# Performance work log

Measured on AMD Instinct MI355X. Metric: run time of the kernel, lower is better.

## Reference

```python
import jax, jax.numpy as jnp
import numpy as np

# SH constants (standard 3DGS eval_sh, degree 3)
C0 = 0.28209479177387814
C1 = 0.4886025119029199
C2 = (1.0925484305920792, -1.0925484305920792, 0.31539156525252005, -1.0925484305920792, 0.5462742152960396)
C3 = (-0.5900435899266435, 2.890611442640554, -0.4570457994644658, 0.3731763325901154, -0.4570457994644658, 1.445305721320277, -0.5900435899266435)

N_GAUSS = 4096
N_PTS = 32768
CHUNK = 4096  # math-identical to torch's 16384 chunking (pure concat of independent points)


def quat_to_rot(q):
    # q: (N,4) normalized, (w,x,y,z) as in 3DGS build_rotation
    r, x, y, z = q[:, 0], q[:, 1], q[:, 2], q[:, 3]
    R = jnp.stack([
        jnp.stack([1 - 2 * (y * y + z * z), 2 * (x * y - r * z), 2 * (x * z + r * y)], -1),
        jnp.stack([2 * (x * y + r * z), 1 - 2 * (x * x + z * z), 2 * (y * z - r * x)], -1),
        jnp.stack([2 * (x * z - r * y), 2 * (y * z + r * x), 1 - 2 * (x * x + y * y)], -1),
    ], axis=-2)  # (N,3,3)
    return R


def eval_sh3(sh, dirs):
    # sh: (N,16) scalar SH coeffs; dirs: (C,N,3) unit directions -> (C,N)
    x, y, z = dirs[..., 0], dirs[..., 1], dirs[..., 2]
    xx, yy, zz = x * x, y * y, z * z
    xy, yz, xz = x * y, y * z, x * z
    s = sh[None]  # (1,N,16)
    res = C0 * s[..., 0]
    res = res - C1 * y * s[..., 1] + C1 * z * s[..., 2] - C1 * x * s[..., 3]
    res = (res + C2[0] * xy * s[..., 4] + C2[1] * yz * s[..., 5]
           + C2[2] * (2 * zz - xx - yy) * s[..., 6]
           + C2[3] * xz * s[..., 7] + C2[4] * (xx - yy) * s[..., 8])
    res = (res + C3[0] * y * (3 * xx - yy) * s[..., 9] + C3[1] * xy * z * s[..., 10]
           + C3[2] * y * (4 * zz - xx - yy) * s[..., 11]
           + C3[3] * z * (2 * zz - 3 * xx - 3 * yy) * s[..., 12]
           + C3[4] * x * (4 * zz - xx - yy) * s[..., 13]
           + C3[5] * z * (xx - yy) * s[..., 14]
           + C3[6] * x * (xx - yy - 3 * zz) * s[..., 15])
    return res


def setup_inputs() -> dict:
    key = jax.random.key(0)
    ks = jax.random.split(key, 9)
    return {
        "network_pts": jax.random.normal(ks[0], (N_PTS, 3), jnp.float32),
        "network_view": jax.random.normal(ks[1], (N_PTS, 3), jnp.float32),
        "network_tx": jax.random.normal(ks[2], (N_PTS, 3), jnp.float32),
        "xyz": jax.random.normal(ks[3], (N_GAUSS, 3), jnp.float32),
        "sh_dc": jax.random.normal(ks[4], (N_GAUSS, 1), jnp.float32),
        "sh_rest": 0.1 * jax.random.normal(ks[5], (N_GAUSS, 15), jnp.float32),
        "scaling": jnp.float32(-3.0) + 0.2 * jax.random.normal(ks[6], (N_GAUSS, 3), jnp.float32),
        "rotation": jax.random.normal(ks[7], (N_GAUSS, 4), jnp.float32),
        "opacity_logit": jax.random.normal(ks[8], (N_GAUSS, 1), jnp.float32),
    }


def reference(network_pts, network_view, network_tx, xyz, sh_dc, sh_rest, scaling, rotation, opacity_logit):
    # activations, matching GaussianModel.setup_functions
    sh = jnp.concatenate([sh_dc, sh_rest], axis=1)            # (N,16)
    s = jnp.exp(scaling)                                      # (N,3)
    q = rotation / jnp.linalg.norm(rotation, axis=1, keepdims=True)
    R = quat_to_rot(q)                                        # (N,3,3)
    # precision = (L L^T)^{-1} with L = R diag(s)  =>  R diag(1/s^2) R^T
    prec = jnp.einsum('nij,nj,nkj->nik', R, 1.0 / (s * s), R)  # (N,3,3)
    op = jax.nn.sigmoid(opacity_logit)[:, 0]                  # (N,)

    pts = network_pts.reshape(-1, CHUNK, 3)

    def chunk_fn(p):  # p: (C,3)
        diff = p[:, None, :] - xyz[None, :, :]                # (C,N,3)
        maha = jnp.einsum('cni,nij,cnj->cn', diff, prec, diff)
        w = op[None, :] * jnp.exp(-0.5 * maha)                # (C,N)
        # dir_pp = xyz - query_point, normalized (as in get_magnitude)
        dirs = -diff / jnp.linalg.norm(diff, axis=-1, keepdims=True)
        mag = jnp.maximum(eval_sh3(sh, dirs), 0.0)            # (C,N)
        return w.sum(axis=1), (w * mag).sum(axis=1)

    opac_c, sig_c = jax.lax.map(chunk_fn, pts)
    return opac_c.reshape(-1), sig_c.reshape(-1)
```

## Files before the change

### kernel.cpp

```cpp
#include <hip/hip_runtime.h>
#include <hip/hip_bf16.h>

#define N_GAUSS 4096
#define N_PTS   32768
#define BLOCK   256
#define NSPLIT  32
#define SEGSZ   (N_GAUSS / NSPLIT)
#define NBLK_PT 128
#define GSTRIDE 32
#define NCELL   4096
#define NBIN    16

#define SH_C0  0.28209479177387814f
#define SH_C1  0.4886025119029199f

#define WS_GP     0
#define WS_GHIST  131072
#define WS_CELLID 135168
#define WS_SPTS   167936
#define WS_ACC    299008
#define WS_HPART  364544

__device__ __forceinline__ int cell_of(float x, float y, float z) {
    int cx = min(15, max(0, (int)((x + 3.2f) * 2.5f)));
    int cy = min(15, max(0, (int)((y + 3.2f) * 2.5f)));
    int cz = min(15, max(0, (int)((z + 3.2f) * 2.5f)));
    int ex = (cx & 1) | ((cx & 2) << 2) | ((cx & 4) << 4) | ((cx & 8) << 6);
    int ey = (cy & 1) | ((cy & 2) << 2) | ((cy & 4) << 4) | ((cy & 8) << 6);
    int ez = (cz & 1) | ((cz & 2) << 2) | ((cz & 4) << 4) | ((cz & 8) << 6);
    return ex | (ey << 1) | (ez << 2);
}

__global__ __launch_bounds__(1024) void binprep_kernel(
    const float* __restrict__ pts, const float* __restrict__ xyz,
    const float* __restrict__ sh_dc, const float* __restrict__ sh_rest,
    const float* __restrict__ scaling, const float* __restrict__ rotation,
    const float* __restrict__ opl, float* __restrict__ gp,
    int* __restrict__ cellid, int* __restrict__ hpart, float* __restrict__ acc)
{
    const int t = threadIdx.x, bx = blockIdx.x;

    if (bx >= 20) {
        float4* a4 = (float4*)acc;
        int base = (bx - 20) * 1024 * 8 + t;
        #pragma unroll
        for (int i = 0; i < 8; ++i) a4[base + i * 1024] = make_float4(0.f, 0.f, 0.f, 0.f);
        return;
    }
    if (bx >= 16) {
        int g = (bx - 16) * 1024 + t;
        float s0 = scaling[3*g+0], s1 = scaling[3*g+1], s2 = scaling[3*g+2];
        float i0 = __expf(-2.0f * s0);
        float i1 = __expf(-2.0f * s1);
        float i2 = __expf(-2.0f * s2);
        float maxs2 = __expf(2.0f * fmaxf(s0, fmaxf(s1, s2)));

        float r = rotation[4*g+0], x = rotation[4*g+1];
        float y = rotation[4*g+2], z = rotation[4*g+3];
        float n = rsqrtf(r*r + x*x + y*y + z*z);
        r *= n; x *= n; y *= n; z *= n;
        float R00 = 1.f - 2.f*(y*y + z*z), R01 = 2.f*(x*y - r*z), R02 = 2.f*(x*z + r*y);
        float R10 = 2.f*(x*y + r*z), R11 = 1.f - 2.f*(x*x + z*z), R12 = 2.f*(y*z - r*x);
        float R20 = 2.f*(x*z - r*y), R21 = 2.f*(y*z + r*x), R22 = 1.f - 2.f*(x*x + y*y);

        float pxx = 0.5f*(R00*R00*i0 + R01*R01*i1 + R02*R02*i2);
        float pxy = 0.5f*(R00*R10*i0 + R01*R11*i1 + R02*R12*i2);
        float pxz = 0.5f*(R00*R20*i0 + R01*R21*i1 + R02*R22*i2);
        float pyy = 0.5f*(R10*R10*i0 + R11*R11*i1 + R12*R12*i2);
        float pyz = 0.5f*(R10*R20*i0 + R11*R21*i1 + R12*R22*i2);
        float pzz = 0.5f*(R20*R20*i0 + R21*R21*i1 + R22*R22*i2);

        float op   = 1.f / (1.f + __expf(-opl[g]));
        float lnop = __logf(op);
        float Tg   = 2.0f * maxs2 * (lnop + 16.0f);

        float* G = gp + (size_t)g * GSTRIDE;
        G[0] = xyz[3*g+0]; G[1] = xyz[3*g+1]; G[2] = xyz[3*g+2]; G[3] = Tg;
        G[4] = pxx; G[5] = pxy; G[6] = pxz; G[7] = pyy;
        G[8] = pyz; G[9] = pzz; G[10] = lnop; G[11] = 0.f;

        const float* sr = sh_rest + (size_t)g * 15;
        G[12] =  SH_C0 * sh_dc[g];
        G[13] = -SH_C1 * sr[0];
        G[14] =  SH_C1 * sr[1];
        G[15] = -SH_C1 * sr[2];
        G[16] =  1.0925484305920792f  * sr[3];
        G[17] = -1.0925484305920792f  * sr[4];
        G[18] =  0.31539156525252005f * sr[5];
        G[19] = -1.0925484305920792f  * sr[6];
        G[20] =  0.5462742152960396f  * sr[7];
        G[21] = -0.5900435899266435f  * sr[8];
        G[22] =  2.890611442640554f   * sr[9];
        G[23] = -0.4570457994644658f  * sr[10];
        G[24] =  0.3731763325901154f  * sr[11];
        G[25] = -0.4570457994644658f  * sr[12];
        G[26] =  1.445305721320277f   * sr[13];
        G[27] = -0.5900435899266435f  * sr[14];
        G[28] = 0.f; G[29] = 0.f; G[30] = 0.f; G[31] = 0.f;
        return;
    }

    __shared__ int s_hist[NCELL];
    #pragma unroll
    for (int i = 0; i < 4; ++i) s_hist[t + i * 1024] = 0;
    __syncthreads();
    #pragma unroll
    for (int k = 0; k < 2; ++k) {
        int p = bx * 2048 + k * 1024 + t;
        float x = pts[3*p+0], y = pts[3*p+1], z = pts[3*p+2];
        int cell = cell_of(x, y, z);
        cellid[p] = cell;
        atomicAdd(&s_hist[cell], 1);
    }
    __syncthreads();
    #pragma unroll
    for (int i = 0; i < 4; ++i) {
        int c = t + i * 1024;
        hpart[bx * NCELL + c] = s_hist[c];
    }
}

__global__ __launch_bounds__(1024) void scan_kernel(
    const int* __restrict__ hpart, int* __restrict__ ghist)
{
    __shared__ int s_scan[1024];
    const int t = threadIdx.x;
    int b = t * 4;
    int c0 = 0, c1 = 0, c2 = 0, c3 = 0;
    #pragma unroll
    for (int k = 0; k < NBIN; ++k) {
        const int* hp = hpart + k * NCELL + b;
        c0 += hp[0]; c1 += hp[1]; c2 += hp[2]; c3 += hp[3];
    }
    int s = c0 + c1 + c2 + c3;
    s_scan[t] = s;
    __syncthreads();
    for (int off = 1; off < 1024; off <<= 1) {
        int v = (t >= off) ? s_scan[t - off] : 0;
        __syncthreads();
        s_scan[t] += v;
        __syncthreads();
    }
    int excl = s_scan[t] - s;
    ghist[b]   = excl;
    ghist[b+1] = excl + c0;
    ghist[b+2] = excl + c0 + c1;
    ghist[b+3] = excl + c0 + c1 + c2;
}

__global__ __launch_bounds__(256) void scatter_kernel(
    const float* __restrict__ pts, const int* __restrict__ cellid,
    int* __restrict__ ghist, float4* __restrict__ spts)
{
    int p = blockIdx.x * 256 + threadIdx.x;
    float x = pts[3*p+0], y = pts[3*p+1], z = pts[3*p+2];
    int pos = atomicAdd(&ghist[cellid[p]], 1);
    spts[pos] = make_float4(x, y, z, __int_as_float(p));
}

__device__ __forceinline__ void eval_one(
    const float4* R, float dx, float dy, float dz, float d2,
    float& opac, float& sig)
{
    float4 q1 = R[1], q2 = R[2];
    float vx = q1.x*dx + q1.y*dy + q1.z*dz;
    float vy = q1.y*dx + q1.w*dy + q2.x*dz;
    float vz = q1.z*dx + q2.x*dy + q2.y*dz;
    float maha = dx*vx + dy*vy + dz*vz;
    float w = __expf(q2.z - maha);
    opac += w;

    if (__any(w > 1e-9f)) {
        float4 q3 = R[3], q4 = R[4], q5 = R[5], q6 = R[6];
        float rinv = rsqrtf(d2);
        float x = -dx * rinv, y = -dy * rinv, z = -dz * rinv;
        float xx = x*x, yy = y*y, zz = z*z;
        float xy = x*y, yz = y*z, xz = x*z;

        float res = q3.x;
        res += y * q3.y;
        res += z * q3.z;
        res += x * q3.w;
        res += xy * q4.x;
        res += yz * q4.y;
        res += (3.f*zz - 1.f) * q4.z;
        res += xz * q4.w;
        float xxmyy = xx - yy;
        res += xxmyy * q5.x;
        res += y * (3.f*xx - yy) * q5.y;
        res += (xy * z) * q5.z;
        float f5z1 = 5.f*zz - 1.f;
        res += y * f5z1 * q5.w;
        res += z * (5.f*zz - 3.f) * q6.x;
        res += x * f5z1 * q6.y;
        res += z * xxmyy * q6.z;
        res += x * (xxmyy - 3.f*zz) * q6.w;

        sig += w * fmaxf(res, 0.f);
    }
}

__global__ __launch_bounds__(BLOCK, 4) void gauss_kernel(
    const float4* __restrict__ spts, const float4* __restrict__ gp4,
    float* __restrict__ acc)
{
    __shared__ float s_min[4][3], s_max[4][3];
    __shared__ int s_nact;
    __shared__ int s_act[SEGSZ];
    __shared__ float4 s_rec[SEGSZ * 8];

    const int tid = threadIdx.x;
    const int pb  = blockIdx.x;
    const int seg = blockIdx.y;
    float4 P = spts[pb * 256 + tid];
    const float px = P.x, py = P.y, pz = P.z;

    float mnx = px, mxx = px, mny = py, mxy = py, mnz = pz, mxz = pz;
    #pragma unroll
    for (int off = 32; off >= 1; off >>= 1) {
        mnx = fminf(mnx, __shfl_xor(mnx, off));
        mxx = fmaxf(mxx, __shfl_xor(mxx, off));
        mny = fminf(mny, __shfl_xor(mny, off));
        mxy = fmaxf(mxy, __shfl_xor(mxy, off));
        mnz = fminf(mnz, __shfl_xor(mnz, off));
        mxz = fmaxf(mxz, __shfl_xor(mxz, off));
    }
    const int wave = tid >> 6;
    if ((tid & 63) == 0) {
        s_min[wave][0] = mnx; s_min[wave][1] = mny; s_min[wave][2] = mnz;
        s_max[wave][0] = mxx; s_max[wave][1] = mxy; s_max[wave][2] = mxz;
    }
    if (tid == 0) s_nact = 0;
    __syncthreads();
    const float bmnx = fminf(fminf(s_min[0][0], s_min[1][0]), fminf(s_min[2][0], s_min[3][0]));
    const float bmny = fminf(fminf(s_min[0][1], s_min[1][1]), fminf(s_min[2][1], s_min[3][1]));
    const float bmnz = fminf(fminf(s_min[0][2], s_min[1][2]), fminf(s_min[2][2], s_min[3][2]));
    const float bmxx = fmaxf(fmaxf(s_max[0][0], s_max[1][0]), fmaxf(s_max[2][0], s_max[3][0]));
    const float bmxy = fmaxf(fmaxf(s_max[0][1], s_max[1][1]), fmaxf(s_max[2][1], s_max[3][1]));
    const float bmxz = fmaxf(fmaxf(s_max[0][2], s_max[1][2]), fmaxf(s_max[2][2], s_max[3][2]));

    if (tid < SEGSZ) {
        const int gg = seg * SEGSZ + tid;
        float4 c = gp4[(size_t)gg << 3];
        float ddx = fmaxf(0.f, fmaxf(bmnx - c.x, c.x - bmxx));
        float ddy = fmaxf(0.f, fmaxf(bmny - c.y, c.y - bmxy));
        float ddz = fmaxf(0.f, fmaxf(bmnz - c.z, c.z - bmxz));
        float dd2 = ddx*ddx + ddy*ddy + ddz*ddz;
        if (dd2 <= c.w) {
            int slot = atomicAdd(&s_nact, 1);
            s_act[slot] = gg;
        }
    }
    __syncthreads();
    const int nact = s_nact;
    if (nact == 0) return;

    for (int idx = tid; idx < nact * 8; idx += BLOCK) {
        int rec = idx >> 3, q = idx & 7;
        s_rec[idx] = gp4[((size_t)s_act[rec] << 3) + q];
    }
    __syncthreads();

    float opac = 0.f, sig = 0.f;
    for (int j = 0; j < nact; j += 2) {
        const bool has1 = (j + 1 < nact);
        const float4* A = &s_rec[j * 8];
        const float4* B = &s_rec[(has1 ? j + 1 : j) * 8];

        float4 aq0 = A[0];
        float4 bq0 = B[0];
        float adx = px - aq0.x, ady = py - aq0.y, adz = pz - aq0.z;
        float bdx = px - bq0.x, bdy = py - bq0.y, bdz = pz - bq0.z;
        float ad2 = adx*adx + ady*ady + adz*adz;
        float bd2 = bdx*bdx + bdy*bdy + bdz*bdz;

        if (!__all(ad2 > aq0.w)) eval_one(A, adx, ady, adz, ad2, opac, sig);
        if (has1 && !__all(bd2 > bq0.w)) eval_one(B, bdx, bdy, bdz, bd2, opac, sig);
    }

    const int pos = pb * 256 + tid;
    atomicAdd(&acc[pos], opac);
    atomicAdd(&acc[N_PTS + pos], sig);
}

__global__ __launch_bounds__(256) void permute_kernel(
    const float* __restrict__ acc, const float4* __restrict__ spts,
    float* __restrict__ out)
{
    int p = blockIdx.x * 256 + threadIdx.x;
    int orig = __float_as_int(spts[p].w);
    out[orig] = acc[p];
    out[N_PTS + orig] = acc[N_PTS + p];
}

extern "C" void kernel_launch(void* const* d_in, const int* in_sizes, int n_in,
                              void* d_out, int out_size, void* d_ws, size_t ws_size,
                              hipStream_t stream) {
    const float* pts      = (const float*)d_in[0];
    const float* xyz      = (const float*)d_in[3];
    const float* sh_dc    = (const float*)d_in[4];
    const float* sh_rest  = (const float*)d_in[5];
    const float* scaling  = (const float*)d_in[6];
    const float* rotation = (const float*)d_in[7];
    const float* opl      = (const float*)d_in[8];

    float*  out    = (float*)d_out;
    float*  wsf    = (float*)d_ws;
    float*  gp     = wsf + WS_GP;
    int*    ghist  = (int*)(wsf + WS_GHIST);
    int*    cellid = (int*)(wsf + WS_CELLID);
    float4* spts   = (float4*)(wsf + WS_SPTS);
    float*  acc    = wsf + WS_ACC;
    int*    hpart  = (int*)(wsf + WS_HPART);

    binprep_kernel<<<dim3(22), dim3(1024), 0, stream>>>(
        pts, xyz, sh_dc, sh_rest, scaling, rotation, opl, gp, cellid, hpart, acc);
    scan_kernel<<<dim3(1), dim3(1024), 0, stream>>>(hpart, ghist);
    scatter_kernel<<<dim3(NBLK_PT), dim3(256), 0, stream>>>(pts, cellid, ghist, spts);

    dim3 grid(NBLK_PT, NSPLIT);
    gauss_kernel<<<grid, dim3(BLOCK), 0, stream>>>(spts, (const float4*)gp, acc);
    permute_kernel<<<dim3(NBLK_PT), dim3(256), 0, stream>>>(acc, spts, out);
}
```

Baseline: 121.0 us.

## Fuse permute into gauss kernel via last-block counter; wave-shuffle scan; halve splits

```diff
diff --git a/kernel.cpp b/kernel.cpp
--- a/kernel.cpp
+++ b/kernel.cpp
@@ -4,12 +4,13 @@
 #define N_GAUSS 4096
 #define N_PTS   32768
 #define BLOCK   256
-#define NSPLIT  32
-#define SEGSZ   (N_GAUSS / NSPLIT)
+#define NSEG    16
+#define SEGG    (N_GAUSS / NSEG)
 #define NBLK_PT 128
 #define GSTRIDE 32
 #define NCELL   4096
 #define NBIN    16
+#define RECCAP  128
 
 #define SH_C0  0.28209479177387814f
 #define SH_C1  0.4886025119029199f
@@ -20,6 +21,7 @@
 #define WS_SPTS   167936
 #define WS_ACC    299008
 #define WS_HPART  364544
+#define WS_DONE   430080
 
 __device__ __forceinline__ int cell_of(float x, float y, float z) {
     int cx = min(15, max(0, (int)((x + 3.2f) * 2.5f)));
@@ -36,7 +38,8 @@
     const float* __restrict__ sh_dc, const float* __restrict__ sh_rest,
     const float* __restrict__ scaling, const float* __restrict__ rotation,
     const float* __restrict__ opl, float* __restrict__ gp,
-    int* __restrict__ cellid, int* __restrict__ hpart, float* __restrict__ acc)
+    int* __restrict__ cellid, int* __restrict__ hpart, float* __restrict__ acc,
+    int* __restrict__ done)
 {
     const int t = threadIdx.x, bx = blockIdx.x;
 
@@ -45,6 +48,7 @@
         int base = (bx - 20) * 1024 * 8 + t;
         #pragma unroll
         for (int i = 0; i < 8; ++i) a4[base + i * 1024] = make_float4(0.f, 0.f, 0.f, 0.f);
+        if (bx == 20 && t < NBLK_PT) done[t] = 0;
         return;
     }
     if (bx >= 16) {
@@ -123,29 +127,44 @@
 __global__ __launch_bounds__(1024) void scan_kernel(
     const int* __restrict__ hpart, int* __restrict__ ghist)
 {
-    __shared__ int s_scan[1024];
+    __shared__ int s_wsum[16];
     const int t = threadIdx.x;
-    int b = t * 4;
-    int c0 = 0, c1 = 0, c2 = 0, c3 = 0;
+    const int lane = t & 63, wv = t >> 6;
+    const int b = t * 4;
+
+    int4 c = make_int4(0, 0, 0, 0);
     #pragma unroll
     for (int k = 0; k < NBIN; ++k) {
-        const int* hp = hpart + k * NCELL + b;
-        c0 += hp[0]; c1 += hp[1]; c2 += hp[2]; c3 += hp[3];
-    }
-    int s = c0 + c1 + c2 + c3;
-    s_scan[t] = s;
-    __syncthreads();
-    for (int off = 1; off < 1024; off <<= 1) {
-        int v = (t >= off) ? s_scan[t - off] : 0;
-        __syncthreads();
-        s_scan[t] += v;
-        __syncthreads();
-    }
-    int excl = s_scan[t] - s;
+        int4 h = *(const int4*)(hpart + k * NCELL + b);
+        c.x += h.x; c.y += h.y; c.z += h.z; c.w += h.w;
+    }
+    int s = c.x + c.y + c.z + c.w;
+
+    int incl = s;
+    #pragma unroll
+    for (int off = 1; off < 64; off <<= 1) {
+        int v = __shfl_up(incl, off);
+        if (lane >= off) incl += v;
+    }
+    if (lane == 63) s_wsum[wv] = incl;
+    __syncthreads();
+    if (wv == 0) {
+        int ws = (lane < 16) ? s_wsum[lane] : 0;
+        int wincl = ws;
+        #pragma unroll
+        for (int off = 1; off < 16; off <<= 1) {
+            int v = __shfl_up(wincl, off);
+            if (lane >= off) wincl += v;
+        }
+        if (lane < 16) s_wsum[lane] = wincl - ws;
+    }
+    __syncthreads();
+
+    int excl = s_wsum[wv] + (incl - s);
     ghist[b]   = excl;
-    ghist[b+1] = excl + c0;
-    ghist[b+2] = excl + c0 + c1;
-    ghist[b+3] = excl + c0 + c1 + c2;
+    ghist[b+1] = excl + c.x;
+    ghist[b+2] = excl + c.x + c.y;
+    ghist[b+3] = excl + c.x + c.y + c.z;
 }
 
 __global__ __launch_bounds__(256) void scatter_kernel(
@@ -202,12 +221,12 @@
 
 __global__ __launch_bounds__(BLOCK, 4) void gauss_kernel(
     const float4* __restrict__ spts, const float4* __restrict__ gp4,
-    float* __restrict__ acc)
+    float* __restrict__ acc, int* __restrict__ done, float* __restrict__ out)
 {
     __shared__ float s_min[4][3], s_max[4][3];
-    __shared__ int s_nact;
-    __shared__ int s_act[SEGSZ];
-    __shared__ float4 s_rec[SEGSZ * 8];
+    __shared__ int s_nact, s_last;
+    __shared__ int s_act[SEGG];
+    __shared__ float4 s_rec[RECCAP * 8];
 
     const int tid = threadIdx.x;
     const int pb  = blockIdx.x;
@@ -239,8 +258,8 @@
     const float bmxy = fmaxf(fmaxf(s_max[0][1], s_max[1][1]), fmaxf(s_max[2][1], s_max[3][1]));
     const float bmxz = fmaxf(fmaxf(s_max[0][2], s_max[1][2]), fmaxf(s_max[2][2], s_max[3][2]));
 
-    if (tid < SEGSZ) {
-        const int gg = seg * SEGSZ + tid;
+    {
+        const int gg = seg * SEGG + tid;
         float4 c = gp4[(size_t)gg << 3];
         float ddx = fmaxf(0.f, fmaxf(bmnx - c.x, c.x - bmxx));
         float ddy = fmaxf(0.f, fmaxf(bmny - c.y, c.y - bmxy));
@@ -253,44 +272,58 @@
     }
     __syncthreads();
     const int nact = s_nact;
-    if (nact == 0) return;
-
-    for (int idx = tid; idx < nact * 8; idx += BLOCK) {
-        int rec = idx >> 3, q = idx & 7;
-        s_rec[idx] = gp4[((size_t)s_act[rec] << 3) + q];
-    }
-    __syncthreads();
 
     float opac = 0.f, sig = 0.f;
-    for (int j = 0; j < nact; j += 2) {
-        const bool has1 = (j + 1 < nact);
-        const float4* A = &s_rec[j * 8];
-        const float4* B = &s_rec[(has1 ? j + 1 : j) * 8];
-
-        float4 aq0 = A[0];
-        float4 bq0 = B[0];
-        float adx = px - aq0.x, ady = py - aq0.y, adz = pz - aq0.z;
-        float bdx = px - bq0.x, bdy = py - bq0.y, bdz = pz - bq0.z;
-        float ad2 = adx*adx + ady*ady + adz*adz;
-        float bd2 = bdx*bdx + bdy*bdy + bdz*bdz;
-
-        if (!__all(ad2 > aq0.w)) eval_one(A, adx, ady, adz, ad2, opac, sig);
-        if (has1 && !__all(bd2 > bq0.w)) eval_one(B, bdx, bdy, bdz, bd2, opac, sig);
+    for (int base = 0; base < nact; base += RECCAP) {
+        const int cnt = min(RECCAP, nact - base);
+        if (base) __syncthreads();
+
+        for (int idx = tid; idx < cnt * 8; idx += BLOCK) {
+            int rec = idx >> 3, q = idx & 7;
+            s_rec[idx] = gp4[((size_t)s_act[base + rec] << 3) + q];
+        }
+        __syncthreads();
+
+        for (int j = 0; j < cnt; j += 2) {
+            const bool has1 = (j + 1 < cnt);
+            const float4* A = &s_rec[j * 8];
+            const float4* B = &s_rec[(has1 ? j + 1 : j) * 8];
+
+            float4 aq0 = A[0];
+            float4 bq0 = B[0];
+            float adx = px - aq0.x, ady = py - aq0.y, adz = pz - aq0.z;
+            float bdx = px - bq0.x, bdy = py - bq0.y, bdz = pz - bq0.z;
+            float ad2 = adx*adx + ady*ady + adz*adz;
+            float bd2 = bdx*bdx + bdy*bdy + bdz*bdz;
+
+            if (!__all(ad2 > aq0.w)) eval_one(A, adx, ady, adz, ad2, opac, sig);
+            if (has1 && !__all(bd2 > bq0.w)) eval_one(B, bdx, bdy, bdz, bd2, opac, sig);
+        }
     }
 
     const int pos = pb * 256 + tid;
-    atomicAdd(&acc[pos], opac);
-    atomicAdd(&acc[N_PTS + pos], sig);
-}
-
-__global__ __launch_bounds__(256) void permute_kernel(
-    const float* __restrict__ acc, const float4* __restrict__ spts,
-    float* __restrict__ out)
-{
-    int p = blockIdx.x * 256 + threadIdx.x;
-    int orig = __float_as_int(spts[p].w);
-    out[orig] = acc[p];
-    out[N_PTS + orig] = acc[N_PTS + p];
+    if (nact) {
+        atomicAdd(&acc[pos], opac);
+        atomicAdd(&acc[N_PTS + pos], sig);
+    }
+
+    __threadfence();
+    __syncthreads();
+    if (tid == 0) {
+        int prev = __hip_atomic_fetch_add(&done[pb], 1, __ATOMIC_ACQ_REL,
+                                          __HIP_MEMORY_SCOPE_AGENT);
+        s_last = (prev == NSEG - 1);
+    }
+    __syncthreads();
+    if (s_last) {
+        float o  = __hip_atomic_load(&acc[pos], __ATOMIC_RELAXED,
+                                     __HIP_MEMORY_SCOPE_AGENT);
+        float sg = __hip_atomic_load(&acc[N_PTS + pos], __ATOMIC_RELAXED,
+                                     __HIP_MEMORY_SCOPE_AGENT);
+        int orig = __float_as_int(P.w);
+        out[orig] = o;
+        out[N_PTS + orig] = sg;
+    }
 }
 
 extern "C" void kernel_launch(void* const* d_in, const int* in_sizes, int n_in,
@@ -312,13 +345,13 @@
     float4* spts   = (float4*)(wsf + WS_SPTS);
     float*  acc    = wsf + WS_ACC;
     int*    hpart  = (int*)(wsf + WS_HPART);
+    int*    done   = (int*)(wsf + WS_DONE);
 
     binprep_kernel<<<dim3(22), dim3(1024), 0, stream>>>(
-        pts, xyz, sh_dc, sh_rest, scaling, rotation, opl, gp, cellid, hpart, acc);
+        pts, xyz, sh_dc, sh_rest, scaling, rotation, opl, gp, cellid, hpart, acc, done);
     scan_kernel<<<dim3(1), dim3(1024), 0, stream>>>(hpart, ghist);
     scatter_kernel<<<dim3(NBLK_PT), dim3(256), 0, stream>>>(pts, cellid, ghist, spts);
 
-    dim3 grid(NBLK_PT, NSPLIT);
-    gauss_kernel<<<grid, dim3(BLOCK), 0, stream>>>(spts, (const float4*)gp, acc);
-    permute_kernel<<<dim3(NBLK_PT), dim3(256), 0, stream>>>(acc, spts, out);
-}
+    dim3 grid(NBLK_PT, NSEG);
+    gauss_kernel<<<grid, dim3(BLOCK), 0, stream>>>(spts, (const float4*)gp, acc, done, out);
+}
```

Result: slower. 251.2 us (+107.6%).
